# Performance work log

Hardware: AMD Instinct MI355X
Metric: run time of the kernel (lower is better)

The kernel has to match this reference:

```python
import jax, jax.numpy as jnp
import numpy as np

N = 100_000
E = 1_600_000
HEADS = 4
HID = 16
OUT = 64
NEG_SLOPE_ATT = 0.2   # PyG GATConv attention leaky_relu
NEG_SLOPE_ACT = 0.01  # F.leaky_relu default between layers


def setup_inputs() -> dict:
    key = jax.random.key(0)
    ks = jax.random.split(key, 16)
    x = jax.random.normal(ks[0], (N, 2), dtype=jnp.float32)
    edge_index = jax.random.randint(ks[1], (2, E), 0, N, dtype=jnp.int64)
    def glorot(k, shape):
        fan = sum(shape[-2:]) if len(shape) >= 2 else shape[-1] * 2
        return jax.random.normal(k, shape, dtype=jnp.float32) * jnp.sqrt(2.0 / fan)
    # layer 0: 2 -> 16 per head, 4 heads, concat
    W0 = glorot(ks[2], (2, HEADS * HID))
    as0 = glorot(ks[3], (HEADS, HID))
    ad0 = glorot(ks[4], (HEADS, HID))
    b0 = jnp.zeros((HEADS * HID,), jnp.float32)
    # layer 1: 64 -> 16 per head, 4 heads, concat
    W1 = glorot(ks[5], (HEADS * HID, HEADS * HID))
    as1 = glorot(ks[6], (HEADS, HID))
    ad1 = glorot(ks[7], (HEADS, HID))
    b1 = jnp.zeros((HEADS * HID,), jnp.float32)
    # layer 2: 64 -> 64, 1 head, no concat
    W2 = glorot(ks[8], (HEADS * HID, OUT))
    as2 = glorot(ks[9], (1, OUT))
    ad2 = glorot(ks[10], (1, OUT))
    b2 = jnp.zeros((OUT,), jnp.float32)
    return {"x": x, "edge_index": edge_index,
            "W0": W0, "as0": as0, "ad0": ad0, "b0": b0,
            "W1": W1, "as1": as1, "ad1": ad1, "b1": b1,
            "W2": W2, "as2": as2, "ad2": ad2, "b2": b2}


def gat_conv(x, src, dst, W, a_src, a_dst, b, heads, out_ch, concat):
    n = x.shape[0]
    h = (x @ W).reshape(n, heads, out_ch)                 # [N,H,C]
    alpha_s = jnp.sum(h * a_src[None], axis=-1)           # [N,H]
    alpha_d = jnp.sum(h * a_dst[None], axis=-1)           # [N,H]
    logits = jax.nn.leaky_relu(alpha_s[src] + alpha_d[dst], NEG_SLOPE_ATT)  # [E,H]
    # segment softmax over edges grouped by target node (self-loops guarantee nonempty)
    m = jax.ops.segment_max(logits, dst, num_segments=n)
    e = jnp.exp(logits - m[dst])
    s = jax.ops.segment_sum(e, dst, num_segments=n)
    alpha = e / s[dst]                                    # [E,H]
    msg = h[src] * alpha[:, :, None]                      # [E,H,C]
    out = jax.ops.segment_sum(msg, dst, num_segments=n)   # [N,H,C]
    out = out.reshape(n, heads * out_ch) if concat else out.mean(axis=1)
    return out + b


def reference(x, edge_index, W0, as0, ad0, b0, W1, as1, ad1, b1, W2, as2, ad2, b2):
    n = x.shape[0]
    loops = jnp.arange(n, dtype=edge_index.dtype)
    src = jnp.concatenate([edge_index[0], loops])  # PyG add_self_loops=True
    dst = jnp.concatenate([edge_index[1], loops])
    h = gat_conv(x, src, dst, W0, as0, ad0, b0, HEADS, HID, True)
    h = jax.nn.leaky_relu(h, NEG_SLOPE_ACT)  # dropout p=0.5 -> identity in eval
    h = gat_conv(h, src, dst, W1, as1, ad1, b1, HEADS, HID, True)
    h = jax.nn.leaky_relu(h, NEG_SLOPE_ACT)
    return gat_conv(h, src, dst, W2, as2, ad2, b2, 1, OUT, False)
```

## Files before the change

### kernel.cpp

```cpp
#include <hip/hip_runtime.h>
#include <hip/hip_bf16.h>


#define LRELU(x, a) fmaxf((x), (a) * (x))
typedef unsigned int u32;
typedef unsigned short u16;

#define NBUCKET 256
#define CAP_A 12288
#define OVCAP 65536

__device__ __forceinline__ float bf2f(u16 v) { return __uint_as_float(((u32)v) << 16); }
__device__ __forceinline__ u16 f2bf(float f) {
    u32 u = __float_as_uint(f);
    return (u16)((u + 0x7FFF + ((u >> 16) & 1)) >> 16);
}

__global__ __launch_bounds__(1024) void k_init(const int* __restrict__ eraw, int e,
                                               int* __restrict__ flag,
                                               const float* __restrict__ W2,
                                               const float* __restrict__ as2,
                                               const float* __restrict__ ad2,
                                               float* __restrict__ va, float* __restrict__ vd) {
    int i = threadIdx.x;
    long long step = (long long)e / 1024;
    if (step == 0) step = 1;
    long long pos = 2LL * (i * step) + 1;
    if (pos < 2LL * e && eraw[pos] != 0) atomicExch(flag, 1);
    if (i < 64) {
        float sa = 0.f, sd = 0.f;
        for (int j = 0; j < 64; j++) {
            float w = W2[i * 64 + j];
            sa += w * as2[j];
            sd += w * ad2[j];
        }
        va[i] = sa;
        vd[i] = sd;
    }
}

#define ACHUNK 2048
__global__ __launch_bounds__(256) void k_passA(const int* __restrict__ eraw, int e, int etot,
                                               const int* __restrict__ flag, int n,
                                               u32* __restrict__ keys, int* __restrict__ gcnt,
                                               int2* __restrict__ ovp, int* __restrict__ ovcnt) {
    __shared__ int bcnt[NBUCKET];
    bcnt[threadIdx.x] = 0;
    __syncthreads();
    const int base = blockIdx.x * ACHUNK;
    const bool i64 = (*flag == 0);
    int s_[8], d_[8], b_[8];
    u32 key_[8];
    #pragma unroll
    for (int j = 0; j < 8; j++) {
        int i = base + j * 256 + threadIdx.x;
        if (i < etot) {
            int s, d;
            if (i < e) {
                if (i64) { s = eraw[2 * i]; d = eraw[2 * (e + i)]; }
                else     { s = eraw[i];     d = eraw[e + i]; }
            } else { s = i - e; d = i - e; }
            s_[j] = s; d_[j] = d;
            int b = (int)(((long long)d * NBUCKET) / n);
            int node_lo_b = (int)(((long long)b * n + NBUCKET - 1) / NBUCKET);
            b_[j] = b;
            key_[j] = (u32)s | ((u32)(d - node_lo_b) << 18);
            atomicAdd(&bcnt[b], 1);
        } else b_[j] = -1;
    }
    __syncthreads();
    {
        int c = bcnt[threadIdx.x];
        bcnt[threadIdx.x] = (c > 0) ? atomicAdd(&gcnt[threadIdx.x], c) : 0;
    }
    __syncthreads();
    #pragma unroll
    for (int j = 0; j < 8; j++) {
        if (b_[j] >= 0) {
            int slot = atomicAdd(&bcnt[b_[j]], 1);
            if (slot < CAP_A) {
                keys[(size_t)b_[j] * CAP_A + slot] = key_[j];
            } else {
                int ov = atomicAdd(ovcnt, 1);
                if (ov < OVCAP) ovp[ov] = make_int2(s_[j], d_[j]);
            }
        }
    }
}

__global__ __launch_bounds__(256) void k_passB(const u32* __restrict__ keys,
                                               const int* __restrict__ gcnt,
                                               const int2* __restrict__ ovp,
                                               const int* __restrict__ ovcnt, int n, int etot,
                                               int* __restrict__ rowstart,
                                               int* __restrict__ csr) {
    __shared__ int lcsr[CAP_A];
    __shared__ int lscan[512];
    __shared__ int lcur[512];
    __shared__ int gscan[NBUCKET];
    const int b = blockIdx.x;
    const int tid = threadIdx.x;
    const int node_lo = (int)(((long long)b * n + NBUCKET - 1) / NBUCKET);
    const int node_hi = (int)(((long long)(b + 1) * n + NBUCKET - 1) / NBUCKET);
    const int nodes = node_hi - node_lo;
    const int cnt_total = gcnt[b];
    const int stored = min(cnt_total, CAP_A);
    const int nov = min(*ovcnt, OVCAP);

    gscan[tid] = gcnt[tid];
    __syncthreads();
    #pragma unroll
    for (int o = 1; o < NBUCKET; o <<= 1) {
        int v = (tid >= o) ? gscan[tid - o] : 0;
        __syncthreads();
        gscan[tid] += v;
        __syncthreads();
    }
    const int bucket_base = (b == 0) ? 0 : gscan[b - 1];

    lscan[tid] = 0; lscan[tid + 256] = 0;
    __syncthreads();
    for (int i = tid; i < stored; i += 256) {
        int dloc = keys[(size_t)b * CAP_A + i] >> 18;
        atomicAdd(&lscan[dloc], 1);
    }
    for (int i = tid; i < nov; i += 256) {
        int d = ovp[i].y;
        if (d >= node_lo && d < node_hi) atomicAdd(&lscan[d - node_lo], 1);
    }
    __syncthreads();
    #pragma unroll
    for (int o = 1; o < 512; o <<= 1) {
        int i0 = tid, i1 = tid + 256;
        int v0 = (i0 >= o) ? lscan[i0 - o] : 0;
        int v1 = (i1 >= o) ? lscan[i1 - o] : 0;
        __syncthreads();
        lscan[i0] += v0; lscan[i1] += v1;
        __syncthreads();
    }
    #pragma unroll
    for (int t = 0; t < 2; t++) {
        int j = tid + t * 256;
        int excl = (j == 0) ? 0 : lscan[j - 1];
        lcur[j] = excl;
        if (j < nodes) rowstart[node_lo + j] = bucket_base + excl;
    }
    if (b == NBUCKET - 1 && tid == 0) rowstart[n] = etot;
    __syncthreads();
    for (int i = tid; i < stored; i += 256) {
        u32 k = keys[(size_t)b * CAP_A + i];
        int slot = atomicAdd(&lcur[k >> 18], 1);
        lcsr[slot] = (int)(k & 0x3FFFFu);
    }
    for (int i = tid; i < nov; i += 256) {
        int2 p = ovp[i];
        if (p.y >= node_lo && p.y < node_hi) {
            int slot = atomicAdd(&lcur[p.y - node_lo], 1);
            lcsr[slot] = p.x;
        }
    }
    __syncthreads();
    for (int i = tid; i < cnt_total; i += 256) csr[bucket_base + i] = lcsr[i];
}

__global__ __launch_bounds__(256) void k_feat0(const float* __restrict__ Xin,
                                               const float* __restrict__ W,
                                               const float* __restrict__ Asrc,
                                               const float* __restrict__ Adst,
                                               u16* __restrict__ Hb, float* __restrict__ asn,
                                               float* __restrict__ adn, int n) {
    const int wv = threadIdx.x >> 6, ln = threadIdx.x & 63;
    const float w0 = W[ln], w1 = W[64 + ln];
    const float a_s = Asrc[ln], a_d = Adst[ln];
    for (int node = blockIdx.x * 4 + wv; node < n; node += gridDim.x * 4) {
        float x0 = Xin[node * 2 + 0], x1 = Xin[node * 2 + 1];
        float acc = fmaf(x1, w1, x0 * w0);
        float ts = acc * a_s, td = acc * a_d;
        #pragma unroll
        for (int o = 1; o < 16; o <<= 1) {
            ts += __shfl_xor(ts, o, 16);
            td += __shfl_xor(td, o, 16);
        }
        Hb[node * 64 + ln] = f2bf(acc);
        if ((ln & 15) == 0) {
            asn[node * 4 + (ln >> 4)] = ts;
            adn[node * 4 + (ln >> 4)] = td;
        }
    }
}

__global__ __launch_bounds__(256) void k_feat64(const float* __restrict__ Xin,
                                                const float* __restrict__ W,
                                                const float* __restrict__ Asrc,
                                                const float* __restrict__ Adst,
                                                u16* __restrict__ Hb, float* __restrict__ asn,
                                                float* __restrict__ adn, int n) {
    __shared__ float Ws[64 * 64];
    __shared__ __align__(16) float Xs[4][256];
    for (int i = threadIdx.x; i < 64 * 64; i += 256) Ws[i] = W[i];
    __syncthreads();
    const int wv = threadIdx.x >> 6, ln = threadIdx.x & 63;
    const float a_s = Asrc[ln], a_d = Adst[ln];
    const int r = ln >> 4;
    const int c4 = (ln & 15) * 4;
    for (int g0 = blockIdx.x * 16 + wv * 4; g0 < n; g0 += gridDim.x * 16) {
        int node_r = g0 + r;
        float4 xq = (node_r < n) ? *(const float4*)&Xin[(size_t)node_r * 64 + c4]
                                 : make_float4(0.f, 0.f, 0.f, 0.f);
        Xs[wv][(c4 + 0) * 4 + r] = xq.x;
        Xs[wv][(c4 + 1) * 4 + r] = xq.y;
        Xs[wv][(c4 + 2) * 4 + r] = xq.z;
        Xs[wv][(c4 + 3) * 4 + r] = xq.w;
        float acc0 = 0.f, acc1 = 0.f, acc2 = 0.f, acc3 = 0.f;
        #pragma unroll 8
        for (int k = 0; k < 64; k++) {
            float w = Ws[k * 64 + ln];
            float4 xk = *(const float4*)&Xs[wv][k * 4];
            acc0 = fmaf(xk.x, w, acc0);
            acc1 = fmaf(xk.y, w, acc1);
            acc2 = fmaf(xk.z, w, acc2);
            acc3 = fmaf(xk.w, w, acc3);
        }
        #pragma unroll
        for (int j = 0; j < 4; j++) {
            int node = g0 + j;
            if (node >= n) break;
            float acc = (j == 0) ? acc0 : (j == 1) ? acc1 : (j == 2) ? acc2 : acc3;
            float ts = acc * a_s, td = acc * a_d;
            #pragma unroll
            for (int o = 1; o < 16; o <<= 1) {
                ts += __shfl_xor(ts, o, 16);
                td += __shfl_xor(td, o, 16);
            }
            Hb[(size_t)node * 64 + ln] = f2bf(acc);
            if ((ln & 15) == 0) {
                asn[node * 4 + (ln >> 4)] = ts;
                adn[node * 4 + (ln >> 4)] = td;
            }
        }
    }
}

#define EDGE_BODY(SRC)                                                        \
    {                                                                         \
        int s_e = (SRC);                                                      \
        float l = LRELU(asn[s_e * HEADS + head] + adme, 0.2f);                \
        float w = __expf(l);                                                  \
        sw += w;                                                              \
        uint4 hv = ((const uint4*)Hb)[s_e * 8 + q];                           \
        v2f w2 = {w, w};                                                      \
        v2f h;                                                                \
        h.x = __uint_as_float(hv.x << 16);                                    \
        h.y = __uint_as_float(hv.x & 0xffff0000u);                            \
        p0 += w2 * h;                                                         \
        h.x = __uint_as_float(hv.y << 16);                                    \
        h.y = __uint_as_float(hv.y & 0xffff0000u);                            \
        p1 += w2 * h;                                                         \
        h.x = __uint_as_float(hv.z << 16);                                    \
        h.y = __uint_as_float(hv.z & 0xffff0000u);                            \
        p2 += w2 * h;                                                         \
        h.x = __uint_as_float(hv.w << 16);                                    \
        h.y = __uint_as_float(hv.w & 0xffff0000u);                            \
        p3 += w2 * h;                                                         \
    }

template <int HEADS, int OUTMODE>
__global__ __launch_bounds__(256) void k_edge(const u16* __restrict__ Hb,
                                              const float* __restrict__ asn,
                                              const float* __restrict__ adn,
                                              const int* __restrict__ rowstart,
                                              const int* __restrict__ csr,
                                              const float* __restrict__ bias,
                                              float4* __restrict__ Outf,
                                              u16* __restrict__ Outb,
                                              const float* __restrict__ va,
                                              const float* __restrict__ vd,
                                              float* __restrict__ asn2,
                                              float* __restrict__ adn2, int n) {
    typedef float v2f __attribute__((ext_vector_type(2)));
    const int wv = threadIdx.x >> 6, ln = threadIdx.x & 63;
    const int node = blockIdx.x * 4 + wv;
    if (node >= n) return;
    const int g = ln >> 3, q = ln & 7;
    const int head = (HEADS == 4) ? (q >> 1) : 0;
    const int start = rowstart[node], end = rowstart[node + 1];
    const int deg = end - start;
    const float adme = adn[node * HEADS + head];

    int sload = (ln < deg) ? csr[start + ln] : 0;

    v2f p0 = {0.f, 0.f}, p1 = {0.f, 0.f}, p2 = {0.f, 0.f}, p3 = {0.f, 0.f};
    float sw = 0.f;
    const int mainE = deg < 64 ? deg : 64;
    const int T = (mainE + 7) >> 3;
    for (int t = 0; t < T; t++) {
        int i = g + 8 * t;
        int s = __shfl(sload, i);
        if (i < mainE) EDGE_BODY(s)
    }
    for (int eg = start + 64 + g; eg < end; eg += 8) EDGE_BODY(csr[eg])

    #pragma unroll
    for (int o = 8; o < 64; o <<= 1) {
        p0.x += __shfl_xor(p0.x, o); p0.y += __shfl_xor(p0.y, o);
        p1.x += __shfl_xor(p1.x, o); p1.y += __shfl_xor(p1.y, o);
        p2.x += __shfl_xor(p2.x, o); p2.y += __shfl_xor(p2.y, o);
        p3.x += __shfl_xor(p3.x, o); p3.y += __shfl_xor(p3.y, o);
        sw += __shfl_xor(sw, o);
    }
    if (ln < 8) {
        const float inv = 1.0f / sw;
        float r0 = p0.x * inv, r1 = p0.y * inv, r2 = p1.x * inv, r3 = p1.y * inv;
        float r4 = p2.x * inv, r5 = p2.y * inv, r6 = p3.x * inv, r7 = p3.y * inv;
        if constexpr (OUTMODE != 2) {
            const float4 bA = ((const float4*)bias)[2 * q];
            const float4 bB = ((const float4*)bias)[2 * q + 1];
            r0 = LRELU(r0 + bA.x, 0.01f); r1 = LRELU(r1 + bA.y, 0.01f);
            r2 = LRELU(r2 + bA.z, 0.01f); r3 = LRELU(r3 + bA.w, 0.01f);
            r4 = LRELU(r4 + bB.x, 0.01f); r5 = LRELU(r5 + bB.y, 0.01f);
            r6 = LRELU(r6 + bB.z, 0.01f); r7 = LRELU(r7 + bB.w, 0.01f);
        }
        if constexpr (OUTMODE == 1) {
            uint4 pb;
            pb.x = (u32)f2bf(r0) | ((u32)f2bf(r1) << 16);
            pb.y = (u32)f2bf(r2) | ((u32)f2bf(r3) << 16);
            pb.z = (u32)f2bf(r4) | ((u32)f2bf(r5) << 16);
            pb.w = (u32)f2bf(r6) | ((u32)f2bf(r7) << 16);
            ((uint4*)Outb)[node * 8 + q] = pb;
            const float4 vA = ((const float4*)va)[2 * q];
            const float4 vB = ((const float4*)va)[2 * q + 1];
            const float4 dA = ((const float4*)vd)[2 * q];
            const float4 dB = ((const float4*)vd)[2 * q + 1];
            float ts = r0 * vA.x + r1 * vA.y + r2 * vA.z + r3 * vA.w +
                       r4 * vB.x + r5 * vB.y + r6 * vB.z + r7 * vB.w;
            float td = r0 * dA.x + r1 * dA.y + r2 * dA.z + r3 * dA.w +
                       r4 * dB.x + r5 * dB.y + r6 * dB.z + r7 * dB.w;
            ts += __shfl_xor(ts, 1, 8); td += __shfl_xor(td, 1, 8);
            ts += __shfl_xor(ts, 2, 8); td += __shfl_xor(td, 2, 8);
            ts += __shfl_xor(ts, 4, 8); td += __shfl_xor(td, 4, 8);
            if (ln == 0) { asn2[node] = ts; adn2[node] = td; }
        } else {
            float4 oA = make_float4(r0, r1, r2, r3);
            float4 oB = make_float4(r4, r5, r6, r7);
            Outf[node * 16 + 2 * q] = oA;
            Outf[node * 16 + 2 * q + 1] = oB;
        }
    }
}

__global__ __launch_bounds__(256) void k_out(const float* __restrict__ Agg,
                                             const float* __restrict__ W2,
                                             const float* __restrict__ b2,
                                             float* __restrict__ Out, int n) {
    __shared__ float Ws[64 * 64];
    __shared__ __align__(16) float Xs[4][256];
    for (int i = threadIdx.x; i < 64 * 64; i += 256) Ws[i] = W2[i];
    __syncthreads();
    const int wv = threadIdx.x >> 6, ln = threadIdx.x & 63;
    const float bb = b2[ln];
    const int r = ln >> 4;
    const int c4 = (ln & 15) * 4;
    for (int g0 = blockIdx.x * 16 + wv * 4; g0 < n; g0 += gridDim.x * 16) {
        int node_r = g0 + r;
        float4 xq = (node_r < n) ? *(const float4*)&Agg[(size_t)node_r * 64 + c4]
                                 : make_float4(0.f, 0.f, 0.f, 0.f);
        Xs[wv][(c4 + 0) * 4 + r] = xq.x;
        Xs[wv][(c4 + 1) * 4 + r] = xq.y;
        Xs[wv][(c4 + 2) * 4 + r] = xq.z;
        Xs[wv][(c4 + 3) * 4 + r] = xq.w;
        float acc0 = 0.f, acc1 = 0.f, acc2 = 0.f, acc3 = 0.f;
        #pragma unroll 8
        for (int k = 0; k < 64; k++) {
            float w = Ws[k * 64 + ln];
            float4 xk = *(const float4*)&Xs[wv][k * 4];
            acc0 = fmaf(xk.x, w, acc0);
            acc1 = fmaf(xk.y, w, acc1);
            acc2 = fmaf(xk.z, w, acc2);
            acc3 = fmaf(xk.w, w, acc3);
        }
        #pragma unroll
        for (int j = 0; j < 4; j++) {
            int node = g0 + j;
            if (node >= n) break;
            float acc = (j == 0) ? acc0 : (j == 1) ? acc1 : (j == 2) ? acc2 : acc3;
            Out[(size_t)node * 64 + ln] = acc + bb;
        }
    }
}

extern "C" void kernel_launch(void* const* d_in, const int* in_sizes, int n_in, void* d_out,
                              int out_size, void* d_ws, size_t ws_size, hipStream_t stream) {
    const float* x = (const float*)d_in[0];
    const int* eraw = (const int*)d_in[1];
    const float* W0 = (const float*)d_in[2];
    const float* as0 = (const float*)d_in[3];
    const float* ad0 = (const float*)d_in[4];
    const float* b0 = (const float*)d_in[5];
    const float* W1 = (const float*)d_in[6];
    const float* as1 = (const float*)d_in[7];
    const float* ad1 = (const float*)d_in[8];
    const float* b1 = (const float*)d_in[9];
    const float* W2 = (const float*)d_in[10];
    const float* as2 = (const float*)d_in[11];
    const float* ad2 = (const float*)d_in[12];
    const float* b2 = (const float*)d_in[13];

    const int n = in_sizes[0] / 2;
    const int e = in_sizes[1] / 2;
    const int etot = e + n;

    char* wp = (char*)d_ws;
    size_t off = 0;
    auto take = [&](size_t bytes) -> void* {
        void* p = wp + off;
        off = (off + bytes + 255) & ~(size_t)255;
        return p;
    };
    size_t hsz = (size_t)n * 64 * 2;
    size_t psz = (size_t)NBUCKET * CAP_A * 4;
    size_t usz = 2 * hsz > psz ? 2 * hsz : psz;
    char* ubase   = (char*)take(usz);
    u16* Hbf      = (u16*)ubase;
    u16* Xb2      = (u16*)(ubase + hsz);
    u32* keys     = (u32*)ubase;
    float* asn    = (float*)take((size_t)n * 4 * 4);
    float* adn    = (float*)take((size_t)n * 4 * 4);
    float* asn2   = (float*)take((size_t)n * 4);
    float* adn2   = (float*)take((size_t)n * 4);
    int* rowstart = (int*)take((size_t)(n + 1) * 4);
    int* gcnt     = (int*)take(NBUCKET * 4);
    int* flag     = (int*)take(256);
    int* ovcnt    = flag + 1;
    float* va     = (float*)take(64 * 4);
    float* vd     = (float*)take(64 * 4);
    int2* ovp     = (int2*)take((size_t)OVCAP * 8);
    int* csr      = (int*)take((size_t)etot * 4);
    (void)ws_size;

    hipMemsetAsync(gcnt, 0, NBUCKET * 4, stream);
    hipMemsetAsync(flag, 0, 256, stream);

    k_init<<<1, 1024, 0, stream>>>(eraw, e, flag, W2, as2, ad2, va, vd);
    k_passA<<<(etot + ACHUNK - 1) / ACHUNK, 256, 0, stream>>>(eraw, e, etot, flag, n, keys,
                                                              gcnt, ovp, ovcnt);
    k_passB<<<NBUCKET, 256, 0, stream>>>(keys, gcnt, ovp, ovcnt, n, etot, rowstart, csr);

    const int nodeBlocks4 = (n + 3) / 4;
    const int gemmBlocks = 2048;
    float* Xact = (float*)d_out;

    k_feat0<<<nodeBlocks4, 256, 0, stream>>>(x, W0, as0, ad0, Hbf, asn, adn, n);
    k_edge<4, 0><<<nodeBlocks4, 256, 0, stream>>>(Hbf, asn, adn, rowstart, csr, b0,
                                                  (float4*)Xact, nullptr, nullptr, nullptr,
                                                  nullptr, nullptr, n);
    k_feat64<<<gemmBlocks, 256, 0, stream>>>(Xact, W1, as1, ad1, Hbf, asn, adn, n);
    k_edge<4, 1><<<nodeBlocks4, 256, 0, stream>>>(Hbf, asn, adn, rowstart, csr, b1,
                                                  nullptr, Xb2, va, vd, asn2, adn2, n);
    k_edge<1, 2><<<nodeBlocks4, 256, 0, stream>>>(Xb2, asn2, adn2, rowstart, csr, nullptr,
                                                  (float4*)Xact, nullptr, nullptr, nullptr,
                                                  nullptr, nullptr, n);
    k_out<<<gemmBlocks, 256, 0, stream>>>(Xact, W2, b2, (float*)d_out, n);
}
```

Baseline: 290.0 us.

## Fuse dense feature transforms into edge aggregation kernels and drop memsets

Folds the 64x64 feature GEMM for layer 1 into the layer-0 edge kernel, and the final W2 projection into the layer-2 edge kernel. Each wave aggregates one node, stages the result in shared memory, and multiplies it by a shared-memory copy of W, using a grid-stride loop over 2048 blocks. This removes the separate GEMM launches and the fp32 intermediate round-trip through global memory. The two hipMemsetAsync calls move into k_init. In exchange, the fused kernels add block-wide __syncthreads inside the node loop, so waves with uneven degrees now wait on each other, and per-block shared memory use rises.

```diff
diff --git a/kernel.cpp b/kernel.cpp
--- a/kernel.cpp
+++ b/kernel.cpp
@@ -10,19 +10,21 @@
 #define CAP_A 12288
 #define OVCAP 65536
 
-__device__ __forceinline__ float bf2f(u16 v) { return __uint_as_float(((u32)v) << 16); }
 __device__ __forceinline__ u16 f2bf(float f) {
     u32 u = __float_as_uint(f);
     return (u16)((u + 0x7FFF + ((u >> 16) & 1)) >> 16);
 }
 
 __global__ __launch_bounds__(1024) void k_init(const int* __restrict__ eraw, int e,
-                                               int* __restrict__ flag,
+                                               int* __restrict__ flag, int* __restrict__ gcnt,
                                                const float* __restrict__ W2,
                                                const float* __restrict__ as2,
                                                const float* __restrict__ ad2,
                                                float* __restrict__ va, float* __restrict__ vd) {
     int i = threadIdx.x;
+    if (i < NBUCKET) gcnt[i] = 0;
+    if (i >= NBUCKET && i < NBUCKET + 2) flag[i - NBUCKET ? 1 : 0] = 0;
+    __syncthreads();
     long long step = (long long)e / 1024;
     if (step == 0) step = 1;
     long long pos = 2LL * (i * step) + 1;
@@ -185,58 +187,6 @@
         if ((ln & 15) == 0) {
             asn[node * 4 + (ln >> 4)] = ts;
             adn[node * 4 + (ln >> 4)] = td;
-        }
-    }
-}
-
-__global__ __launch_bounds__(256) void k_feat64(const float* __restrict__ Xin,
-                                                const float* __restrict__ W,
-                                                const float* __restrict__ Asrc,
-                                                const float* __restrict__ Adst,
-                                                u16* __restrict__ Hb, float* __restrict__ asn,
-                                                float* __restrict__ adn, int n) {
-    __shared__ float Ws[64 * 64];
-    __shared__ __align__(16) float Xs[4][256];
-    for (int i = threadIdx.x; i < 64 * 64; i += 256) Ws[i] = W[i];
-    __syncthreads();
-    const int wv = threadIdx.x >> 6, ln = threadIdx.x & 63;
-    const float a_s = Asrc[ln], a_d = Adst[ln];
-    const int r = ln >> 4;
-    const int c4 = (ln & 15) * 4;
-    for (int g0 = blockIdx.x * 16 + wv * 4; g0 < n; g0 += gridDim.x * 16) {
-        int node_r = g0 + r;
-        float4 xq = (node_r < n) ? *(const float4*)&Xin[(size_t)node_r * 64 + c4]
-                                 : make_float4(0.f, 0.f, 0.f, 0.f);
-        Xs[wv][(c4 + 0) * 4 + r] = xq.x;
-        Xs[wv][(c4 + 1) * 4 + r] = xq.y;
-        Xs[wv][(c4 + 2) * 4 + r] = xq.z;
-        Xs[wv][(c4 + 3) * 4 + r] = xq.w;
-        float acc0 = 0.f, acc1 = 0.f, acc2 = 0.f, acc3 = 0.f;
-        #pragma unroll 8
-        for (int k = 0; k < 64; k++) {
-            float w = Ws[k * 64 + ln];
-            float4 xk = *(const float4*)&Xs[wv][k * 4];
-            acc0 = fmaf(xk.x, w, acc0);
-            acc1 = fmaf(xk.y, w, acc1);
-            acc2 = fmaf(xk.z, w, acc2);
-            acc3 = fmaf(xk.w, w, acc3);
-        }
-        #pragma unroll
-        for (int j = 0; j < 4; j++) {
-            int node = g0 + j;
-            if (node >= n) break;
-            float acc = (j == 0) ? acc0 : (j == 1) ? acc1 : (j == 2) ? acc2 : acc3;
-            float ts = acc * a_s, td = acc * a_d;
-            #pragma unroll
-            for (int o = 1; o < 16; o <<= 1) {
-                ts += __shfl_xor(ts, o, 16);
-                td += __shfl_xor(td, o, 16);
-            }
-            Hb[(size_t)node * 64 + ln] = f2bf(acc);
-            if ((ln & 15) == 0) {
-                asn[node * 4 + (ln >> 4)] = ts;
-                adn[node * 4 + (ln >> 4)] = td;
-            }
         }
     }
 }
@@ -271,119 +221,138 @@
                                               const int* __restrict__ rowstart,
                                               const int* __restrict__ csr,
                                               const float* __restrict__ bias,
-                                              float4* __restrict__ Outf,
+                                              const float* __restrict__ Wt,
+                                              const float* __restrict__ ats,
+                                              const float* __restrict__ atd,
+                                              u16* __restrict__ outHb,
+                                              float* __restrict__ outAsn,
+                                              float* __restrict__ outAdn,
                                               u16* __restrict__ Outb,
                                               const float* __restrict__ va,
                                               const float* __restrict__ vd,
                                               float* __restrict__ asn2,
-                                              float* __restrict__ adn2, int n) {
+                                              float* __restrict__ adn2,
+                                              float* __restrict__ OutF, int n) {
     typedef float v2f __attribute__((ext_vector_type(2)));
+    constexpr bool COOP = (OUTMODE != 1);
+    __shared__ float Ws[COOP ? 4096 : 1];
+    __shared__ __align__(16) float Xs[COOP ? 4 : 1][COOP ? 64 : 1];
+    if constexpr (COOP) {
+        for (int i = threadIdx.x; i < 4096; i += 256) Ws[i] = Wt[i];
+        __syncthreads();
+    }
     const int wv = threadIdx.x >> 6, ln = threadIdx.x & 63;
-    const int node = blockIdx.x * 4 + wv;
-    if (node >= n) return;
     const int g = ln >> 3, q = ln & 7;
     const int head = (HEADS == 4) ? (q >> 1) : 0;
-    const int start = rowstart[node], end = rowstart[node + 1];
-    const int deg = end - start;
-    const float adme = adn[node * HEADS + head];
-
-    int sload = (ln < deg) ? csr[start + ln] : 0;
-
-    v2f p0 = {0.f, 0.f}, p1 = {0.f, 0.f}, p2 = {0.f, 0.f}, p3 = {0.f, 0.f};
-    float sw = 0.f;
-    const int mainE = deg < 64 ? deg : 64;
-    const int T = (mainE + 7) >> 3;
-    for (int t = 0; t < T; t++) {
-        int i = g + 8 * t;
-        int s = __shfl(sload, i);
-        if (i < mainE) EDGE_BODY(s)
-    }
-    for (int eg = start + 64 + g; eg < end; eg += 8) EDGE_BODY(csr[eg])
-
-    #pragma unroll
-    for (int o = 8; o < 64; o <<= 1) {
-        p0.x += __shfl_xor(p0.x, o); p0.y += __shfl_xor(p0.y, o);
-        p1.x += __shfl_xor(p1.x, o); p1.y += __shfl_xor(p1.y, o);
-        p2.x += __shfl_xor(p2.x, o); p2.y += __shfl_xor(p2.y, o);
-        p3.x += __shfl_xor(p3.x, o); p3.y += __shfl_xor(p3.y, o);
-        sw += __shfl_xor(sw, o);
-    }
-    if (ln < 8) {
+
+    for (int base = blockIdx.x * 4; base < n; base += gridDim.x * 4) {
+        const int node = base + wv;
+        const bool valid = node < n;
+
+        int start = 0, end = 0;
+        float adme = 0.f;
+        if (valid) {
+            start = rowstart[node];
+            end = rowstart[node + 1];
+            adme = adn[node * HEADS + head];
+        }
+        const int deg = end - start;
+        int sload = (ln < deg) ? csr[start + ln] : 0;
+
+        v2f p0 = {0.f, 0.f}, p1 = {0.f, 0.f}, p2 = {0.f, 0.f}, p3 = {0.f, 0.f};
+        float sw = 0.f;
+        const int mainE = deg < 64 ? deg : 64;
+        const int T = (mainE + 7) >> 3;
+        for (int t = 0; t < T; t++) {
+            int i = g + 8 * t;
+            int s = __shfl(sload, i);
+            if (i < mainE) EDGE_BODY(s)
+        }
+        for (int eg = start + 64 + g; eg < end; eg += 8) EDGE_BODY(csr[eg])
+
+        #pragma unroll
+        for (int o = 8; o < 64; o <<= 1) {
+            p0.x += __shfl_xor(p0.x, o); p0.y += __shfl_xor(p0.y, o);
+            p1.x += __shfl_xor(p1.x, o); p1.y += __shfl_xor(p1.y, o);
+            p2.x += __shfl_xor(p2.x, o); p2.y += __shfl_xor(p2.y, o);
+            p3.x += __shfl_xor(p3.x, o); p3.y += __shfl_xor(p3.y, o);
+            sw += __shfl_xor(sw, o);
+        }
         const float inv = 1.0f / sw;
         float r0 = p0.x * inv, r1 = p0.y * inv, r2 = p1.x * inv, r3 = p1.y * inv;
         float r4 = p2.x * inv, r5 = p2.y * inv, r6 = p3.x * inv, r7 = p3.y * inv;
-        if constexpr (OUTMODE != 2) {
-            const float4 bA = ((const float4*)bias)[2 * q];
-            const float4 bB = ((const float4*)bias)[2 * q + 1];
-            r0 = LRELU(r0 + bA.x, 0.01f); r1 = LRELU(r1 + bA.y, 0.01f);
-            r2 = LRELU(r2 + bA.z, 0.01f); r3 = LRELU(r3 + bA.w, 0.01f);
-            r4 = LRELU(r4 + bB.x, 0.01f); r5 = LRELU(r5 + bB.y, 0.01f);
-            r6 = LRELU(r6 + bB.z, 0.01f); r7 = LRELU(r7 + bB.w, 0.01f);
-        }
+
         if constexpr (OUTMODE == 1) {
-            uint4 pb;
-            pb.x = (u32)f2bf(r0) | ((u32)f2bf(r1) << 16);
-            pb.y = (u32)f2bf(r2) | ((u32)f2bf(r3) << 16);
-            pb.z = (u32)f2bf(r4) | ((u32)f2bf(r5) << 16);
-            pb.w = (u32)f2bf(r6) | ((u32)f2bf(r7) << 16);
-            ((uint4*)Outb)[node * 8 + q] = pb;
-            const float4 vA = ((const float4*)va)[2 * q];
-            const float4 vB = ((const float4*)va)[2 * q + 1];
-            const float4 dA = ((const float4*)vd)[2 * q];
-            const float4 dB = ((const float4*)vd)[2 * q + 1];
-            float ts = r0 * vA.x + r1 * vA.y + r2 * vA.z + r3 * vA.w +
-                       r4 * vB.x + r5 * vB.y + r6 * vB.z + r7 * vB.w;
-            float td = r0 * dA.x + r1 * dA.y + r2 * dA.z + r3 * dA.w +
-                       r4 * dB.x + r5 * dB.y + r6 * dB.z + r7 * dB.w;
-            ts += __shfl_xor(ts, 1, 8); td += __shfl_xor(td, 1, 8);
-            ts += __shfl_xor(ts, 2, 8); td += __shfl_xor(td, 2, 8);
-            ts += __shfl_xor(ts, 4, 8); td += __shfl_xor(td, 4, 8);
-            if (ln == 0) { asn2[node] = ts; adn2[node] = td; }
+            if (valid && ln < 8) {
+                const float4 bA = ((const float4*)bias)[2 * q];
+                const float4 bB = ((const float4*)bias)[2 * q + 1];
+                r0 = LRELU(r0 + bA.x, 0.01f); r1 = LRELU(r1 + bA.y, 0.01f);
+                r2 = LRELU(r2 + bA.z, 0.01f); r3 = LRELU(r3 + bA.w, 0.01f);
+                r4 = LRELU(r4 + bB.x, 0.01f); r5 = LRELU(r5 + bB.y, 0.01f);
+                r6 = LRELU(r6 + bB.z, 0.01f); r7 = LRELU(r7 + bB.w, 0.01f);
+                uint4 pb;
+                pb.x = (u32)f2bf(r0) | ((u32)f2bf(r1) << 16);
+                pb.y = (u32)f2bf(r2) | ((u32)f2bf(r3) << 16);
+                pb.z = (u32)f2bf(r4) | ((u32)f2bf(r5) << 16);
+                pb.w = (u32)f2bf(r6) | ((u32)f2bf(r7) << 16);
+                ((uint4*)Outb)[node * 8 + q] = pb;
+                const float4 vA = ((const float4*)va)[2 * q];
+                const float4 vB = ((const float4*)va)[2 * q + 1];
+                const float4 dA = ((const float4*)vd)[2 * q];
+                const float4 dB = ((const float4*)vd)[2 * q + 1];
+                float ts = r0 * vA.x + r1 * vA.y + r2 * vA.z + r3 * vA.w +
+                           r4 * vB.x + r5 * vB.y + r6 * vB.z + r7 * vB.w;
+                float td = r0 * dA.x + r1 * dA.y + r2 * dA.z + r3 * dA.w +
+                           r4 * dB.x + r5 * dB.y + r6 * dB.z + r7 * dB.w;
+                ts += __shfl_xor(ts, 1, 8); td += __shfl_xor(td, 1, 8);
+                ts += __shfl_xor(ts, 2, 8); td += __shfl_xor(td, 2, 8);
+                ts += __shfl_xor(ts, 4, 8); td += __shfl_xor(td, 4, 8);
+                if (ln == 0) { asn2[node] = ts; adn2[node] = td; }
+            }
         } else {
-            float4 oA = make_float4(r0, r1, r2, r3);
-            float4 oB = make_float4(r4, r5, r6, r7);
-            Outf[node * 16 + 2 * q] = oA;
-            Outf[node * 16 + 2 * q + 1] = oB;
-        }
-    }
-}
-
-__global__ __launch_bounds__(256) void k_out(const float* __restrict__ Agg,
-                                             const float* __restrict__ W2,
-                                             const float* __restrict__ b2,
-                                             float* __restrict__ Out, int n) {
-    __shared__ float Ws[64 * 64];
-    __shared__ __align__(16) float Xs[4][256];
-    for (int i = threadIdx.x; i < 64 * 64; i += 256) Ws[i] = W2[i];
-    __syncthreads();
-    const int wv = threadIdx.x >> 6, ln = threadIdx.x & 63;
-    const float bb = b2[ln];
-    const int r = ln >> 4;
-    const int c4 = (ln & 15) * 4;
-    for (int g0 = blockIdx.x * 16 + wv * 4; g0 < n; g0 += gridDim.x * 16) {
-        int node_r = g0 + r;
-        float4 xq = (node_r < n) ? *(const float4*)&Agg[(size_t)node_r * 64 + c4]
-                                 : make_float4(0.f, 0.f, 0.f, 0.f);
-        Xs[wv][(c4 + 0) * 4 + r] = xq.x;
-        Xs[wv][(c4 + 1) * 4 + r] = xq.y;
-        Xs[wv][(c4 + 2) * 4 + r] = xq.z;
-        Xs[wv][(c4 + 3) * 4 + r] = xq.w;
-        float acc0 = 0.f, acc1 = 0.f, acc2 = 0.f, acc3 = 0.f;
-        #pragma unroll 8
-        for (int k = 0; k < 64; k++) {
-            float w = Ws[k * 64 + ln];
-            float4 xk = *(const float4*)&Xs[wv][k * 4];
-            acc0 = fmaf(xk.x, w, acc0);
-            acc1 = fmaf(xk.y, w, acc1);
-            acc2 = fmaf(xk.z, w, acc2);
-            acc3 = fmaf(xk.w, w, acc3);
-        }
-        #pragma unroll
-        for (int j = 0; j < 4; j++) {
-            int node = g0 + j;
-            if (node >= n) break;
-            float acc = (j == 0) ? acc0 : (j == 1) ? acc1 : (j == 2) ? acc2 : acc3;
-            Out[(size_t)node * 64 + ln] = acc + bb;
+            if constexpr (OUTMODE == 0) {
+                const float4 bA = ((const float4*)bias)[2 * q];
+                const float4 bB = ((const float4*)bias)[2 * q + 1];
+                r0 = LRELU(r0 + bA.x, 0.01f); r1 = LRELU(r1 + bA.y, 0.01f);
+                r2 = LRELU(r2 + bA.z, 0.01f); r3 = LRELU(r3 + bA.w, 0.01f);
+                r4 = LRELU(r4 + bB.x, 0.01f); r5 = LRELU(r5 + bB.y, 0.01f);
+                r6 = LRELU(r6 + bB.z, 0.01f); r7 = LRELU(r7 + bB.w, 0.01f);
+            }
+            if (valid && ln < 8) {
+                float* xr = &Xs[wv][8 * ln];
+                xr[0] = r0; xr[1] = r1; xr[2] = r2; xr[3] = r3;
+                xr[4] = r4; xr[5] = r5; xr[6] = r6; xr[7] = r7;
+            }
+            __syncthreads();
+            float acc = 0.f;
+            if (valid) {
+                #pragma unroll
+                for (int k4 = 0; k4 < 16; k4++) {
+                    float4 xk = *(const float4*)&Xs[wv][k4 * 4];
+                    acc = fmaf(xk.x, Ws[(4 * k4 + 0) * 64 + ln], acc);
+                    acc = fmaf(xk.y, Ws[(4 * k4 + 1) * 64 + ln], acc);
+                    acc = fmaf(xk.z, Ws[(4 * k4 + 2) * 64 + ln], acc);
+                    acc = fmaf(xk.w, Ws[(4 * k4 + 3) * 64 + ln], acc);
+                }
+            }
+            __syncthreads();
+            if (valid) {
+                if constexpr (OUTMODE == 0) {
+                    float ts = acc * ats[ln], td = acc * atd[ln];
+                    #pragma unroll
+                    for (int o = 1; o < 16; o <<= 1) {
+                        ts += __shfl_xor(ts, o, 16);
+                        td += __shfl_xor(td, o, 16);
+                    }
+                    outHb[(size_t)node * 64 + ln] = f2bf(acc);
+                    if ((ln & 15) == 0) {
+                        outAsn[node * 4 + (ln >> 4)] = ts;
+                        outAdn[node * 4 + (ln >> 4)] = td;
+                    }
+                } else {
+                    OutF[(size_t)node * 64 + ln] = acc + bias[ln];
+                }
+            }
         }
     }
 }
@@ -420,11 +389,13 @@
     size_t psz = (size_t)NBUCKET * CAP_A * 4;
     size_t usz = 2 * hsz > psz ? 2 * hsz : psz;
     char* ubase   = (char*)take(usz);
-    u16* Hbf      = (u16*)ubase;
-    u16* Xb2      = (u16*)(ubase + hsz);
+    u16* A        = (u16*)ubase;
+    u16* B        = (u16*)(ubase + hsz);
     u32* keys     = (u32*)ubase;
-    float* asn    = (float*)take((size_t)n * 4 * 4);
-    float* adn    = (float*)take((size_t)n * 4 * 4);
+    float* asn0   = (float*)take((size_t)n * 4 * 4);
+    float* adn0   = (float*)take((size_t)n * 4 * 4);
+    float* asn1   = (float*)take((size_t)n * 4 * 4);
+    float* adn1   = (float*)take((size_t)n * 4 * 4);
     float* asn2   = (float*)take((size_t)n * 4);
     float* adn2   = (float*)take((size_t)n * 4);
     int* rowstart = (int*)take((size_t)(n + 1) * 4);
@@ -437,27 +408,23 @@
     int* csr      = (int*)take((size_t)etot * 4);
     (void)ws_size;
 
-    hipMemsetAsync(gcnt, 0, NBUCKET * 4, stream);
-    hipMemsetAsync(flag, 0, 256, stream);
-
-    k_init<<<1, 1024, 0, stream>>>(eraw, e, flag, W2, as2, ad2, va, vd);
+    k_init<<<1, 1024, 0, stream>>>(eraw, e, flag, gcnt, W2, as2, ad2, va, vd);
     k_passA<<<(etot + ACHUNK - 1) / ACHUNK, 256, 0, stream>>>(eraw, e, etot, flag, n, keys,
                                                               gcnt, ovp, ovcnt);
     k_passB<<<NBUCKET, 256, 0, stream>>>(keys, gcnt, ovp, ovcnt, n, etot, rowstart, csr);
 
     const int nodeBlocks4 = (n + 3) / 4;
-    const int gemmBlocks = 2048;
-    float* Xact = (float*)d_out;
-
-    k_feat0<<<nodeBlocks4, 256, 0, stream>>>(x, W0, as0, ad0, Hbf, asn, adn, n);
-    k_edge<4, 0><<<nodeBlocks4, 256, 0, stream>>>(Hbf, asn, adn, rowstart, csr, b0,
-                                                  (float4*)Xact, nullptr, nullptr, nullptr,
-                                                  nullptr, nullptr, n);
-    k_feat64<<<gemmBlocks, 256, 0, stream>>>(Xact, W1, as1, ad1, Hbf, asn, adn, n);
-    k_edge<4, 1><<<nodeBlocks4, 256, 0, stream>>>(Hbf, asn, adn, rowstart, csr, b1,
-                                                  nullptr, Xb2, va, vd, asn2, adn2, n);
-    k_edge<1, 2><<<nodeBlocks4, 256, 0, stream>>>(Xb2, asn2, adn2, rowstart, csr, nullptr,
-                                                  (float4*)Xact, nullptr, nullptr, nullptr,
-                                                  nullptr, nullptr, n);
-    k_out<<<gemmBlocks, 256, 0, stream>>>(Xact, W2, b2, (float*)d_out, n);
-}
+    const int coopBlocks = 2048;
+
+    k_feat0<<<nodeBlocks4, 256, 0, stream>>>(x, W0, as0, ad0, A, asn0, adn0, n);
+    k_edge<4, 0><<<coopBlocks, 256, 0, stream>>>(A, asn0, adn0, rowstart, csr, b0, W1, as1,
+                                                 ad1, B, asn1, adn1, nullptr, nullptr,
+                                                 nullptr, nullptr, nullptr, nullptr, n);
+    k_edge<4, 1><<<nodeBlocks4, 256, 0, stream>>>(B, asn1, adn1, rowstart, csr, b1, nullptr,
+                                                  nullptr, nullptr, nullptr, nullptr, nullptr,
+                                                  A, va, vd, asn2, adn2, nullptr, n);
+    k_edge<1, 2><<<coopBlocks, 256, 0, stream>>>(A, asn2, adn2, rowstart, csr, b2, W2, nullptr,
+                                                 nullptr, nullptr, nullptr, nullptr, nullptr,
+                                                 nullptr, nullptr, nullptr, nullptr,
+                                                 (float*)d_out, n);
+}
```

Measured after the change: 318.5 us. 1.1x slower.
